# Kernel tuning notes

Measured on AMD Instinct MI355X. Metric: run time of the kernel, lower is better.

## Reference

```python
import jax, jax.numpy as jnp
import numpy as np

N_TOKENS = 16384
INPUT_DIM = 4096
N_EXPERTS = 64
TOP_K = 8
EPS = 1e-12  # torch F.normalize eps
SCALE = 5.0


def l2_normalize(v):
    # matches torch.nn.functional.normalize(p=2, dim=-1, eps=1e-12)
    norm = jnp.sqrt(jnp.sum(v * v, axis=-1, keepdims=True))
    return v / jnp.maximum(norm, EPS)


def setup_inputs() -> dict:
    key = jax.random.key(0)
    kx, ks = jax.random.split(key)
    x = jax.random.normal(kx, (N_TOKENS, INPUT_DIM), dtype=jnp.float32)
    # signatures are L2-normalized in the module (_normalize_signatures)
    sig = jax.random.normal(ks, (N_EXPERTS, INPUT_DIM), dtype=jnp.float32)
    phase_signatures = l2_normalize(sig)
    return {"x": x, "phase_signatures": phase_signatures}


def reference(x, phase_signatures):
    x_norm = l2_normalize(x)                                   # [N, D]
    resonance = jnp.einsum('nd,ed->ne', x_norm, phase_signatures)  # [N, E]
    resonance = resonance * SCALE
    k = min(TOP_K, resonance.shape[-1])
    top_k_resonance, top_k_indices = jax.lax.top_k(resonance, k)   # [N, k]
    weights = jax.nn.softplus(top_k_resonance)                 # [N, k]
    return (weights, top_k_indices, resonance)
```

## Files before the change

### kernel.cpp

```cpp
#include <hip/hip_runtime.h>
#include <cmath>


#define N_TOKENS 16384
#define DIM      4096
#define NE       64
#define TOPK     8
#define SCALE    5.0f
#define EPS      1e-12f
#define NS       32

typedef short  frag   __attribute__((ext_vector_type(8)));
typedef float  f32x16 __attribute__((ext_vector_type(16)));
typedef int    i32x4  __attribute__((ext_vector_type(4)));

__device__ __forceinline__ void split3(float v, unsigned& h1, unsigned& h2, unsigned& h3) {
    unsigned u  = __builtin_bit_cast(unsigned, v);
    unsigned r1 = (u + 0x7FFFu + ((u >> 16) & 1u)) & 0xFFFF0000u;
    float    d1 = v - __builtin_bit_cast(float, r1);
    unsigned w  = __builtin_bit_cast(unsigned, d1);
    unsigned r2 = (w + 0x7FFFu + ((w >> 16) & 1u)) & 0xFFFF0000u;
    float    d2 = d1 - __builtin_bit_cast(float, r2);
    unsigned z  = __builtin_bit_cast(unsigned, d2);
    unsigned r3 = (z + 0x7FFFu + ((z >> 16) & 1u)) & 0xFFFF0000u;
    h1 = r1 >> 16; h2 = r2 >> 16; h3 = r3 >> 16;
}

__launch_bounds__(256)
__global__ void convert_sig(const float* __restrict__ sig,
                            short* __restrict__ h1,
                            short* __restrict__ h2,
                            short* __restrict__ h3) {
    const int tid  = blockIdx.x * 256 + threadIdx.x;
    const int lane = tid & 63;
    const int kb   = (tid >> 6) & 255;
    const int tile = tid >> 14;
    const int e31  = lane & 31, hf = lane >> 5;
    const float* src = sig + (size_t)(tile * 32 + e31) * DIM + kb * 16 + hf * 8;
    const float4 v0 = *(const float4*)(src);
    const float4 v1 = *(const float4*)(src + 4);
    const float vs[8] = {v0.x, v0.y, v0.z, v0.w, v1.x, v1.y, v1.z, v1.w};
    frag o1, o2, o3;
#pragma unroll
    for (int p = 0; p < 8; ++p) {
        unsigned a, b, c;
        split3(vs[p], a, b, c);
        o1[p] = (short)a; o2[p] = (short)b; o3[p] = (short)c;
    }
    const int base = ((tile * 256 + kb) * 64 + lane) * 8;
    *(frag*)(h1 + base) = o1;
    *(frag*)(h2 + base) = o2;
    *(frag*)(h3 + base) = o3;
}

__launch_bounds__(512, 4)
__global__ void gemm_fused(const float* __restrict__ x,
                           const short* __restrict__ sh1,
                           const short* __restrict__ sh2,
                           const short* __restrict__ sh3,
                           float* __restrict__ outR,
                           float* __restrict__ outW,
                           float* __restrict__ outI) {
    __shared__ float red[4][64][34];
    __shared__ float res[32][68];
    __shared__ float sqred[8][32];
    __shared__ float scl[32];

    const int t    = threadIdx.x;
    const int lane = t & 63;
    const int w    = t >> 6;
    const int l31  = lane & 31;
    const int half = lane >> 5;

    const int tb = blockIdx.x * 32;
    const int k0 = w * (DIM / 8);

    const float* ap = x + (size_t)(tb + l31) * DIM + k0 + 8 * half;
    const int bbase = ((w * NS) * 64 + lane) * 8;
    const short* b1p = sh1 + bbase;
    const short* b2p = sh2 + bbase;
    const short* b3p = sh3 + bbase;
    const int TILE1 = 256 * 64 * 8;

    f32x16 c0 = {};
    f32x16 c1 = {};
    float sq = 0.f;

    float4 cur0 = *(const float4*)(ap);
    float4 cur1 = *(const float4*)(ap + 4);
    float4 nxt0 = *(const float4*)(ap + 16);
    float4 nxt1 = *(const float4*)(ap + 20);

#pragma unroll 1
    for (int st = 0; st < NS; ++st) {
        const frag b1a = *(const frag*)(b1p);
        const frag b1b = *(const frag*)(b1p + TILE1);
        const frag b2a = *(const frag*)(b2p);
        const frag b2b = *(const frag*)(b2p + TILE1);
        const frag b3a = *(const frag*)(b3p);
        const frag b3b = *(const frag*)(b3p + TILE1);

        float4 f0 = cur0, f1 = cur1;
        if (st + 2 < NS) {
            f0 = *(const float4*)(ap + 32);
            f1 = *(const float4*)(ap + 36);
        }

        const float vals[8] = {cur0.x, cur0.y, cur0.z, cur0.w,
                               cur1.x, cur1.y, cur1.z, cur1.w};
        i32x4 a1i, a2i, a3i;
#pragma unroll
        for (int p = 0; p < 4; ++p) {
            const float v0 = vals[2 * p], v1 = vals[2 * p + 1];
            sq = fmaf(v0, v0, sq);
            sq = fmaf(v1, v1, sq);
            unsigned h10, h20, h30, h11, h21, h31;
            split3(v0, h10, h20, h30);
            split3(v1, h11, h21, h31);
            a1i[p] = (int)(h10 | (h11 << 16));
            a2i[p] = (int)(h20 | (h21 << 16));
            a3i[p] = (int)(h30 | (h31 << 16));
        }
        const frag A1 = __builtin_bit_cast(frag, a1i);
        const frag A2 = __builtin_bit_cast(frag, a2i);
        const frag A3 = __builtin_bit_cast(frag, a3i);

        c0 = __builtin_amdgcn_mfma_f32_32x32x16_bf16(A1, b1a, c0, 0, 0, 0);
        c1 = __builtin_amdgcn_mfma_f32_32x32x16_bf16(A1, b1b, c1, 0, 0, 0);
        c0 = __builtin_amdgcn_mfma_f32_32x32x16_bf16(A1, b2a, c0, 0, 0, 0);
        c1 = __builtin_amdgcn_mfma_f32_32x32x16_bf16(A1, b2b, c1, 0, 0, 0);
        c0 = __builtin_amdgcn_mfma_f32_32x32x16_bf16(A2, b1a, c0, 0, 0, 0);
        c1 = __builtin_amdgcn_mfma_f32_32x32x16_bf16(A2, b1b, c1, 0, 0, 0);
        c0 = __builtin_amdgcn_mfma_f32_32x32x16_bf16(A1, b3a, c0, 0, 0, 0);
        c1 = __builtin_amdgcn_mfma_f32_32x32x16_bf16(A1, b3b, c1, 0, 0, 0);
        c0 = __builtin_amdgcn_mfma_f32_32x32x16_bf16(A3, b1a, c0, 0, 0, 0);
        c1 = __builtin_amdgcn_mfma_f32_32x32x16_bf16(A3, b1b, c1, 0, 0, 0);
        c0 = __builtin_amdgcn_mfma_f32_32x32x16_bf16(A2, b2a, c0, 0, 0, 0);
        c1 = __builtin_amdgcn_mfma_f32_32x32x16_bf16(A2, b2b, c1, 0, 0, 0);

        cur0 = nxt0; cur1 = nxt1; nxt0 = f0; nxt1 = f1;
        ap += 16; b1p += 512; b2p += 512; b3p += 512;
    }

    sq += __shfl_xor(sq, 32);
    if (lane < 32) sqred[w][l31] = sq;

    if (w >= 4) {
#pragma unroll
        for (int r = 0; r < 16; ++r) {
            red[w - 4][lane][r]      = c0[r];
            red[w - 4][lane][16 + r] = c1[r];
        }
    }
    __syncthreads();

    if (t < 32) {
        float q = 0.f;
#pragma unroll
        for (int ww = 0; ww < 8; ++ww) q += sqred[ww][t];
        scl[t] = SCALE / fmaxf(sqrtf(q), EPS);
    }

    if (w < 4) {
#pragma unroll
        for (int r = 0; r < 16; ++r) {
            red[w][lane][r]      = c0[r] + red[w][lane][r];
            red[w][lane][16 + r] = c1[r] + red[w][lane][16 + r];
        }
    }
    __syncthreads();

    const int wm = w & 3, tile = w >> 2;
    const int et = l31 + 32 * tile;
#pragma unroll
    for (int j = 0; j < 4; ++j) {
        const int R = 4 * w + j;
        const float a = red[0][lane][R] + red[1][lane][R] +
                        red[2][lane][R] + red[3][lane][R];
        const int token = j + 8 * wm + 4 * half;
        res[token][et] = a * scl[token];
    }
    __syncthreads();

    {
        const int token = t >> 4, q4 = (t & 15) * 4;
        *(float4*)(outR + (size_t)(tb + token) * NE + q4) =
            *(const float4*)(&res[token][q4]);
    }

#pragma unroll 1
    for (int tt = 0; tt < 4; ++tt) {
        const int token = 4 * w + tt;
        const float v = res[token][lane];
        const unsigned u = __builtin_bit_cast(unsigned, v);
        const unsigned s = u ^ ((unsigned)(((int)u) >> 31) | 0x80000000u);
        unsigned long long cur = ((unsigned long long)s << 32) | (unsigned)(63 - lane);

        float bw = 0.f;
        int   bi = 0;
#pragma unroll
        for (int m = 0; m < TOPK; ++m) {
            unsigned long long r = cur;
#pragma unroll
            for (int d = 32; d >= 1; d >>= 1) {
                const unsigned long long o = __shfl_xor(r, d);
                r = (o > r) ? o : r;
            }
            const int we = 63 - (int)(r & 63ull);
            const float bv = __shfl(v, we);
            if (lane == we) cur = 0ull;
            if (lane == m) { bw = bv; bi = we; }
        }
        if (lane < TOPK) {
            const size_t ob = (size_t)(tb + token) * TOPK + lane;
            outW[ob] = log1pf(expf(bw));
            outI[ob] = (float)bi;
        }
    }
}

extern "C" void kernel_launch(void* const* d_in, const int* in_sizes, int n_in,
                              void* d_out, int out_size, void* d_ws, size_t ws_size,
                              hipStream_t stream) {
    const float* x   = (const float*)d_in[0];
    const float* sig = (const float*)d_in[1];
    float* out  = (float*)d_out;
    float* outW = out;
    float* outI = out + (size_t)N_TOKENS * TOPK;
    float* outR = out + (size_t)N_TOKENS * TOPK * 2;

    const size_t SIGE = (size_t)NE * DIM;
    short* sh1 = (short*)d_ws;
    short* sh2 = sh1 + SIGE;
    short* sh3 = sh2 + SIGE;

    convert_sig<<<128, 256, 0, stream>>>(sig, sh1, sh2, sh3);
    gemm_fused<<<N_TOKENS / 32, 512, 0, stream>>>(x, sh1, sh2, sh3, outR, outW, outI);
}
```

Measured before the change: 396.6 us.

## Stage x slabs into LDS via async global_load_lds with double buffering

Replaces per-wave strided global loads of x (each wave reading a distinct K range) with cooperative, coalesced 128-column slab loads into LDS using global_load_lds, double-buffered, with XOR swizzle to avoid bank conflicts. Each wave now covers a K sub-range within every slab, and the B fragment walk is remapped to match. The goal is better coalescing of x reads across the 32-row tile. The cost is a __syncthreads per slab iteration (32 barriers) and LDS traffic that shares storage with the reduction buffers.

```diff
diff --git a/kernel.cpp b/kernel.cpp
--- a/kernel.cpp
+++ b/kernel.cpp
@@ -8,7 +8,7 @@
 #define TOPK     8
 #define SCALE    5.0f
 #define EPS      1e-12f
-#define NS       32
+#define NSLAB    32
 
 typedef short  frag   __attribute__((ext_vector_type(8)));
 typedef float  f32x16 __attribute__((ext_vector_type(16)));
@@ -53,6 +53,26 @@
     *(frag*)(h3 + base) = o3;
 }
 
+__device__ __forceinline__ void stage_slab(const float* __restrict__ x, int tb,
+                                           int c0, float* slabbuf, int w, int lane) {
+    const int i1 = w * 64 + lane;
+    const int r1 = i1 >> 5;
+    const int j1 = (i1 & 31) ^ (r1 & 7);
+    const float* g1 = x + (size_t)(tb + r1) * DIM + c0 + 4 * j1;
+    const int i2 = i1 + 512;
+    const int r2 = i2 >> 5;
+    const int j2 = (i2 & 31) ^ (r2 & 7);
+    const float* g2 = x + (size_t)(tb + r2) * DIM + c0 + 4 * j2;
+    float* l1 = slabbuf + w * 256;
+    float* l2 = slabbuf + w * 256 + 2048;
+    __builtin_amdgcn_global_load_lds(
+        (const __attribute__((address_space(1))) void*)g1,
+        (__attribute__((address_space(3))) void*)l1, 16, 0, 0);
+    __builtin_amdgcn_global_load_lds(
+        (const __attribute__((address_space(1))) void*)g2,
+        (__attribute__((address_space(3))) void*)l2, 16, 0, 0);
+}
+
 __launch_bounds__(512, 4)
 __global__ void gemm_fused(const float* __restrict__ x,
                            const short* __restrict__ sh1,
@@ -61,10 +81,12 @@
                            float* __restrict__ outR,
                            float* __restrict__ outW,
                            float* __restrict__ outI) {
-    __shared__ float red[4][64][34];
-    __shared__ float res[32][68];
-    __shared__ float sqred[8][32];
-    __shared__ float scl[32];
+    __shared__ __align__(16) char smem[45056];
+    float* slab = (float*)smem;
+    float (*red)[64][34] = (float(*)[64][34])smem;
+    float (*res)[68]     = (float(*)[68])(smem + 34816);
+    float (*sqred)[32]   = (float(*)[32])(smem + 43520);
+    float* scl           = (float*)(smem + 44544);
 
     const int t    = threadIdx.x;
     const int lane = t & 63;
@@ -73,26 +95,31 @@
     const int half = lane >> 5;
 
     const int tb = blockIdx.x * 32;
-    const int k0 = w * (DIM / 8);
-
-    const float* ap = x + (size_t)(tb + l31) * DIM + k0 + 8 * half;
-    const int bbase = ((w * NS) * 64 + lane) * 8;
-    const short* b1p = sh1 + bbase;
-    const short* b2p = sh2 + bbase;
-    const short* b3p = sh3 + bbase;
+
+    const short* b1p = sh1 + ((size_t)(w * 64) + lane) * 8;
+    const short* b2p = sh2 + ((size_t)(w * 64) + lane) * 8;
+    const short* b3p = sh3 + ((size_t)(w * 64) + lane) * 8;
     const int TILE1 = 256 * 64 * 8;
 
     f32x16 c0 = {};
     f32x16 c1 = {};
     float sq = 0.f;
 
-    float4 cur0 = *(const float4*)(ap);
-    float4 cur1 = *(const float4*)(ap + 4);
-    float4 nxt0 = *(const float4*)(ap + 16);
-    float4 nxt1 = *(const float4*)(ap + 20);
+    const int kk = 4 * w + 2 * half;
+    const int rr = l31;
+    const int roff = rr * 128;
+    const int sl0 = (kk ^ (rr & 7)) * 4;
+    const int sl1 = ((kk + 1) ^ (rr & 7)) * 4;
+
+    stage_slab(x, tb, 0, slab, w, lane);
+    __syncthreads();
 
 #pragma unroll 1
-    for (int st = 0; st < NS; ++st) {
+    for (int s = 0; s < NSLAB; ++s) {
+        const int b = s & 1;
+        if (s + 1 < NSLAB)
+            stage_slab(x, tb, (s + 1) * 128, slab + (1 - b) * 4096, w, lane);
+
         const frag b1a = *(const frag*)(b1p);
         const frag b1b = *(const frag*)(b1p + TILE1);
         const frag b2a = *(const frag*)(b2p);
@@ -100,14 +127,11 @@
         const frag b3a = *(const frag*)(b3p);
         const frag b3b = *(const frag*)(b3p + TILE1);
 
-        float4 f0 = cur0, f1 = cur1;
-        if (st + 2 < NS) {
-            f0 = *(const float4*)(ap + 32);
-            f1 = *(const float4*)(ap + 36);
-        }
-
-        const float vals[8] = {cur0.x, cur0.y, cur0.z, cur0.w,
-                               cur1.x, cur1.y, cur1.z, cur1.w};
+        const float* base = slab + b * 4096 + roff;
+        const float4 va = *(const float4*)(base + sl0);
+        const float4 vb = *(const float4*)(base + sl1);
+
+        const float vals[8] = {va.x, va.y, va.z, va.w, vb.x, vb.y, vb.z, vb.w};
         i32x4 a1i, a2i, a3i;
 #pragma unroll
         for (int p = 0; p < 4; ++p) {
@@ -138,8 +162,8 @@
         c0 = __builtin_amdgcn_mfma_f32_32x32x16_bf16(A2, b2a, c0, 0, 0, 0);
         c1 = __builtin_amdgcn_mfma_f32_32x32x16_bf16(A2, b2b, c1, 0, 0, 0);
 
-        cur0 = nxt0; cur1 = nxt1; nxt0 = f0; nxt1 = f1;
-        ap += 16; b1p += 512; b2p += 512; b3p += 512;
+        b1p += 4096; b2p += 4096; b3p += 4096;
+        __syncthreads();
     }
 
     sq += __shfl_xor(sq, 32);
@@ -193,8 +217,8 @@
         const int token = 4 * w + tt;
         const float v = res[token][lane];
         const unsigned u = __builtin_bit_cast(unsigned, v);
-        const unsigned s = u ^ ((unsigned)(((int)u) >> 31) | 0x80000000u);
-        unsigned long long cur = ((unsigned long long)s << 32) | (unsigned)(63 - lane);
+        const unsigned sbits = u ^ ((unsigned)(((int)u) >> 31) | 0x80000000u);
+        unsigned long long cur = ((unsigned long long)sbits << 32) | (unsigned)(63 - lane);
 
         float bw = 0.f;
         int   bi = 0;
```

After: 386.4 us. 1.03x faster.
